# Kernel optimization log

Measured on AMD Instinct MI355X. Metric: run time of the kernel, lower is better.

Reference implementation:

```python
import jax, jax.numpy as jnp
import numpy as np

NUM_THRESH = 1000


def setup_inputs() -> dict:
    key = jax.random.key(0)
    k1, k2 = jax.random.split(key)
    B, C, H, W = 16, 4, 512, 512
    inp = jax.random.uniform(k1, (B, C, H, W), dtype=jnp.float32)
    targ = (jax.random.uniform(k2, (B, C, H, W)) < 0.3).astype(jnp.float32)
    return {"input": inp, "target": targ}


def _max_f1_loss(input, target):
    # input, target: [B, C, H, W]; loss = mean_c (1 - max_t F1_c(t))
    B, C, H, W = input.shape
    N = B * H * W
    x = jnp.transpose(input, (1, 0, 2, 3)).reshape(C, N)   # [C, N]
    y = jnp.transpose(target, (1, 0, 2, 3)).reshape(C, N)  # [C, N]
    thresholds = jnp.linspace(0.0, 1.0, NUM_THRESH).astype(jnp.float32)

    def per_class(xc, yc):
        # idx[n] = number of thresholds strictly below xc[n]  (in [0, 1000])
        # sample n is predicted positive (xc > t_k) exactly for k < idx[n]
        idx = jnp.searchsorted(thresholds, xc, side='left')
        s_y = jax.ops.segment_sum(yc, idx, num_segments=NUM_THRESH + 1)
        s_1 = jax.ops.segment_sum(jnp.ones_like(yc), idx, num_segments=NUM_THRESH + 1)
        cum_y = jnp.cumsum(s_y)[:NUM_THRESH]  # sum of y over samples with idx <= k
        cum_1 = jnp.cumsum(s_1)[:NUM_THRESH]
        total_y = jnp.sum(yc)
        TP = total_y - cum_y            # sum(target * pred) per threshold
        PP = jnp.float32(N) - cum_1     # sum(pred) per threshold
        FP = PP - TP                    # sum((1-target) * pred)
        FN = total_y - TP               # sum(target * (1-pred))
        denom = TP + (FN + FP) * 0.5
        F1 = jnp.where(denom == 0, 0.0, TP / jnp.where(denom == 0, 1.0, denom))
        return 1.0 - jnp.max(F1)

    losses = jax.vmap(per_class)(x, y)  # [C]
    return jnp.mean(losses)


def reference(input, target):
    return _max_f1_loss(input, target)
```

## Files before the change

kernel.cpp:

```cpp
#include <hip/hip_runtime.h>

#define NBINS 1001
#define HIST_BLOCK 256
#define ELEMS_PER_BLOCK 16384

__device__ __forceinline__ int bin_of(float v) {
    double d = ceil((double)v * 999.0);
    int k = (int)d;
    if (k < 0) k = 0;
    if (k > 1000) k = 1000;
    return k;
}

__global__ __launch_bounds__(HIST_BLOCK) void hist_kernel(
    const float* __restrict__ x, const float* __restrict__ y,
    unsigned long long* __restrict__ ghist, int HW, int C)
{
    __shared__ unsigned long long lh[NBINS];
    const int tid = threadIdx.x;
    for (int i = tid; i < NBINS; i += HIST_BLOCK) lh[i] = 0ULL;
    __syncthreads();

    const long long start = (long long)blockIdx.x * ELEMS_PER_BLOCK;
    const int c = (int)((start / HW) % C);

    const float4* __restrict__ x4 = (const float4*)(x + start);
    const float4* __restrict__ y4 = (const float4*)(y + start);
    const int nvec = ELEMS_PER_BLOCK >> 2;

    for (int i = tid; i < nvec; i += HIST_BLOCK) {
        float4 xv = x4[i];
        float4 yv = y4[i];
        {
            int b = bin_of(xv.x);
            unsigned long long add = 1ULL + ((yv.x > 0.5f) ? (1ULL << 32) : 0ULL);
            atomicAdd(&lh[b], add);
        }
        {
            int b = bin_of(xv.y);
            unsigned long long add = 1ULL + ((yv.y > 0.5f) ? (1ULL << 32) : 0ULL);
            atomicAdd(&lh[b], add);
        }
        {
            int b = bin_of(xv.z);
            unsigned long long add = 1ULL + ((yv.z > 0.5f) ? (1ULL << 32) : 0ULL);
            atomicAdd(&lh[b], add);
        }
        {
            int b = bin_of(xv.w);
            unsigned long long add = 1ULL + ((yv.w > 0.5f) ? (1ULL << 32) : 0ULL);
            atomicAdd(&lh[b], add);
        }
    }
    __syncthreads();

    unsigned long long* gh = ghist + (size_t)c * NBINS;
    for (int i = tid; i < NBINS; i += HIST_BLOCK) {
        unsigned long long v = lh[i];
        if (v) atomicAdd(&gh[i], v);
    }
}

__global__ __launch_bounds__(1024) void f1_kernel(
    const unsigned long long* __restrict__ ghist, float* __restrict__ out, int C)
{
    __shared__ unsigned long long sbuf[1024];
    __shared__ float smax[1024];
    const int tid = threadIdx.x;
    float loss_sum = 0.0f;

    for (int c = 0; c < C; ++c) {
        unsigned long long v = (tid < NBINS) ? ghist[(size_t)c * NBINS + tid] : 0ULL;
        sbuf[tid] = v;
        __syncthreads();
        #pragma unroll
        for (int off = 1; off < 1024; off <<= 1) {
            unsigned long long t = (tid >= off) ? sbuf[tid - off] : 0ULL;
            __syncthreads();
            sbuf[tid] += t;
            __syncthreads();
        }
        unsigned long long tot = sbuf[NBINS - 1];
        unsigned int total_cnt = (unsigned int)(tot & 0xffffffffULL);
        unsigned int total_y   = (unsigned int)(tot >> 32);

        float f1 = 0.0f;
        if (tid < NBINS - 1) {
            unsigned long long cum = sbuf[tid];
            unsigned int cnt_cum = (unsigned int)(cum & 0xffffffffULL);
            unsigned int y_cum   = (unsigned int)(cum >> 32);
            unsigned int TP = total_y - y_cum;
            unsigned int PP = total_cnt - cnt_cum;
            unsigned int denom = total_y + PP;
            f1 = (denom == 0u) ? 0.0f : (2.0f * (float)TP) / (float)denom;
        }
        smax[tid] = f1;
        __syncthreads();
        #pragma unroll
        for (int s = 512; s > 0; s >>= 1) {
            if (tid < s) smax[tid] = fmaxf(smax[tid], smax[tid + s]);
            __syncthreads();
        }
        loss_sum += 1.0f - smax[0];
        __syncthreads();
    }

    if (tid == 0) out[0] = loss_sum / (float)C;
}

extern "C" void kernel_launch(void* const* d_in, const int* in_sizes, int n_in,
                              void* d_out, int out_size, void* d_ws, size_t ws_size,
                              hipStream_t stream) {
    const float* x = (const float*)d_in[0];
    const float* y = (const float*)d_in[1];
    float* out = (float*)d_out;

    const int B = 16, C = 4, H = 512, W = 512;
    const int HW = H * W;
    const long long total = (long long)in_sizes[0];

    unsigned long long* ghist = (unsigned long long*)d_ws;

    hipMemsetAsync(d_ws, 0, (size_t)C * NBINS * sizeof(unsigned long long), stream);

    const int nblocks = (int)(total / ELEMS_PER_BLOCK);
    hist_kernel<<<nblocks, HIST_BLOCK, 0, stream>>>(x, y, ghist, HW, C);
    f1_kernel<<<1, 1024, 0, stream>>>(ghist, out, C);
    (void)B; (void)n_in; (void)out_size; (void)ws_size;
}
```

Before: 161.7 us.

## Pack shared histogram into 32-bit bins and use wave-shuffle scan in F1 kernel

The shared-memory histogram now uses 32-bit atomics, holding count in the low 16 bits and positives in the high 16 bits, instead of 64-bit atomics. Elements per block are halved so per-bin counts fit in 16 bits, and the fixed 8 float4 loads per thread are unrolled. The F1 kernel drops the barrier-heavy shared-memory Hillis-Steele scan and tree max. It handles all four classes at once with wavefront shuffle scans and reductions. The trade-off is twice as many blocks doing global atomic flushes, and the code now assumes C=4 and a fixed block size.

```diff
diff --git a/kernel.cpp b/kernel.cpp
--- a/kernel.cpp
+++ b/kernel.cpp
@@ -2,7 +2,7 @@
 
 #define NBINS 1001
 #define HIST_BLOCK 256
-#define ELEMS_PER_BLOCK 16384
+#define ELEMS_PER_BLOCK 8192
 
 __device__ __forceinline__ int bin_of(float v) {
     double d = ceil((double)v * 999.0);
@@ -16,9 +16,9 @@
     const float* __restrict__ x, const float* __restrict__ y,
     unsigned long long* __restrict__ ghist, int HW, int C)
 {
-    __shared__ unsigned long long lh[NBINS];
+    __shared__ unsigned int lh[NBINS];
     const int tid = threadIdx.x;
-    for (int i = tid; i < NBINS; i += HIST_BLOCK) lh[i] = 0ULL;
+    for (int i = tid; i < NBINS; i += HIST_BLOCK) lh[i] = 0u;
     __syncthreads();
 
     const long long start = (long long)blockIdx.x * ELEMS_PER_BLOCK;
@@ -26,67 +26,87 @@
 
     const float4* __restrict__ x4 = (const float4*)(x + start);
     const float4* __restrict__ y4 = (const float4*)(y + start);
-    const int nvec = ELEMS_PER_BLOCK >> 2;
 
-    for (int i = tid; i < nvec; i += HIST_BLOCK) {
-        float4 xv = x4[i];
-        float4 yv = y4[i];
-        {
-            int b = bin_of(xv.x);
-            unsigned long long add = 1ULL + ((yv.x > 0.5f) ? (1ULL << 32) : 0ULL);
-            atomicAdd(&lh[b], add);
-        }
-        {
-            int b = bin_of(xv.y);
-            unsigned long long add = 1ULL + ((yv.y > 0.5f) ? (1ULL << 32) : 0ULL);
-            atomicAdd(&lh[b], add);
-        }
-        {
-            int b = bin_of(xv.z);
-            unsigned long long add = 1ULL + ((yv.z > 0.5f) ? (1ULL << 32) : 0ULL);
-            atomicAdd(&lh[b], add);
-        }
-        {
-            int b = bin_of(xv.w);
-            unsigned long long add = 1ULL + ((yv.w > 0.5f) ? (1ULL << 32) : 0ULL);
-            atomicAdd(&lh[b], add);
-        }
+    #pragma unroll
+    for (int ii = 0; ii < 4; ++ii) {
+        const int i0 = (ii * 2)     * HIST_BLOCK + tid;
+        const int i1 = (ii * 2 + 1) * HIST_BLOCK + tid;
+        float4 xa = x4[i0];
+        float4 ya = y4[i0];
+        float4 xb = x4[i1];
+        float4 yb = y4[i1];
+        atomicAdd(&lh[bin_of(xa.x)], 1u + ((ya.x > 0.5f) ? 0x10000u : 0u));
+        atomicAdd(&lh[bin_of(xa.y)], 1u + ((ya.y > 0.5f) ? 0x10000u : 0u));
+        atomicAdd(&lh[bin_of(xa.z)], 1u + ((ya.z > 0.5f) ? 0x10000u : 0u));
+        atomicAdd(&lh[bin_of(xa.w)], 1u + ((ya.w > 0.5f) ? 0x10000u : 0u));
+        atomicAdd(&lh[bin_of(xb.x)], 1u + ((yb.x > 0.5f) ? 0x10000u : 0u));
+        atomicAdd(&lh[bin_of(xb.y)], 1u + ((yb.y > 0.5f) ? 0x10000u : 0u));
+        atomicAdd(&lh[bin_of(xb.z)], 1u + ((yb.z > 0.5f) ? 0x10000u : 0u));
+        atomicAdd(&lh[bin_of(xb.w)], 1u + ((yb.w > 0.5f) ? 0x10000u : 0u));
     }
     __syncthreads();
 
     unsigned long long* gh = ghist + (size_t)c * NBINS;
     for (int i = tid; i < NBINS; i += HIST_BLOCK) {
-        unsigned long long v = lh[i];
-        if (v) atomicAdd(&gh[i], v);
+        unsigned int v = lh[i];
+        if (v) {
+            unsigned long long add = (unsigned long long)(v & 0xffffu)
+                                   | ((unsigned long long)(v >> 16) << 32);
+            atomicAdd(&gh[i], add);
+        }
     }
 }
 
 __global__ __launch_bounds__(1024) void f1_kernel(
     const unsigned long long* __restrict__ ghist, float* __restrict__ out, int C)
 {
-    __shared__ unsigned long long sbuf[1024];
-    __shared__ float smax[1024];
-    const int tid = threadIdx.x;
-    float loss_sum = 0.0f;
+    __shared__ unsigned long long wtot[4][16];
+    __shared__ float wmax[4][16];
+    const int tid  = threadIdx.x;
+    const int lane = tid & 63;
+    const int wave = tid >> 6;
 
-    for (int c = 0; c < C; ++c) {
-        unsigned long long v = (tid < NBINS) ? ghist[(size_t)c * NBINS + tid] : 0ULL;
-        sbuf[tid] = v;
-        __syncthreads();
+    unsigned long long v[4];
+    #pragma unroll
+    for (int c = 0; c < 4; ++c)
+        v[c] = (tid < NBINS) ? ghist[(size_t)c * NBINS + tid] : 0ULL;
+
+    #pragma unroll
+    for (int off = 1; off < 64; off <<= 1) {
         #pragma unroll
-        for (int off = 1; off < 1024; off <<= 1) {
-            unsigned long long t = (tid >= off) ? sbuf[tid - off] : 0ULL;
-            __syncthreads();
-            sbuf[tid] += t;
-            __syncthreads();
+        for (int c = 0; c < 4; ++c) {
+            unsigned long long t = __shfl_up(v[c], off, 64);
+            if (lane >= off) v[c] += t;
         }
-        unsigned long long tot = sbuf[NBINS - 1];
+    }
+    if (lane == 63) {
+        #pragma unroll
+        for (int c = 0; c < 4; ++c) wtot[c][wave] = v[c];
+    }
+    __syncthreads();
+
+    if (wave == 0) {
+        const int c = lane >> 4, w = lane & 15;
+        unsigned long long t = wtot[c][w];
+        #pragma unroll
+        for (int off = 1; off < 16; off <<= 1) {
+            unsigned long long s = __shfl_up(t, off, 16);
+            if (w >= off) t += s;
+        }
+        wtot[c][w] = t;
+    }
+    __syncthreads();
+
+    float m[4];
+    #pragma unroll
+    for (int c = 0; c < 4; ++c) {
+        unsigned long long cum = v[c];
+        if (wave > 0) cum += wtot[c][wave - 1];
+        unsigned long long tot = wtot[c][15];
         unsigned int total_cnt = (unsigned int)(tot & 0xffffffffULL);
         unsigned int total_y   = (unsigned int)(tot >> 32);
-
         float f1 = 0.0f;
         if (tid < NBINS - 1) {
-            unsigned long long cum = sbuf[tid];
             unsigned int cnt_cum = (unsigned int)(cum & 0xffffffffULL);
             unsigned int y_cum   = (unsigned int)(cum >> 32);
             unsigned int TP = total_y - y_cum;
@@ -94,18 +114,32 @@
             unsigned int denom = total_y + PP;
             f1 = (denom == 0u) ? 0.0f : (2.0f * (float)TP) / (float)denom;
         }
-        smax[tid] = f1;
-        __syncthreads();
-        #pragma unroll
-        for (int s = 512; s > 0; s >>= 1) {
-            if (tid < s) smax[tid] = fmaxf(smax[tid], smax[tid + s]);
-            __syncthreads();
-        }
-        loss_sum += 1.0f - smax[0];
-        __syncthreads();
+        m[c] = f1;
     }
 
-    if (tid == 0) out[0] = loss_sum / (float)C;
+    #pragma unroll
+    for (int off = 32; off > 0; off >>= 1) {
+        #pragma unroll
+        for (int c = 0; c < 4; ++c)
+            m[c] = fmaxf(m[c], __shfl_down(m[c], off, 64));
+    }
+    if (lane == 0) {
+        #pragma unroll
+        for (int c = 0; c < 4; ++c) wmax[c][wave] = m[c];
+    }
+    __syncthreads();
+
+    if (tid == 0) {
+        float loss = 0.0f;
+        #pragma unroll
+        for (int c = 0; c < 4; ++c) {
+            float mm = wmax[c][0];
+            #pragma unroll
+            for (int w = 1; w < 16; ++w) mm = fmaxf(mm, wmax[c][w]);
+            loss += 1.0f - mm;
+        }
+        out[0] = loss * 0.25f;
+    }
 }
 
 extern "C" void kernel_launch(void* const* d_in, const int* in_sizes, int n_in,
@@ -115,7 +149,7 @@
     const float* y = (const float*)d_in[1];
     float* out = (float*)d_out;
 
-    const int B = 16, C = 4, H = 512, W = 512;
+    const int C = 4, H = 512, W = 512;
     const int HW = H * W;
     const long long total = (long long)in_sizes[0];
 
@@ -126,5 +160,5 @@
     const int nblocks = (int)(total / ELEMS_PER_BLOCK);
     hist_kernel<<<nblocks, HIST_BLOCK, 0, stream>>>(x, y, ghist, HW, C);
     f1_kernel<<<1, 1024, 0, stream>>>(ghist, out, C);
-    (void)B; (void)n_in; (void)out_size; (void)ws_size;
+    (void)n_in; (void)out_size; (void)ws_size;
 }
```

Result: faster. 151.3 us (-6.4%).
